# Kernel tuning notes

Measured on AMD Instinct MI355X. Metric: run time of the kernel, lower is better.

The kernel has to match this reference:

```python
import jax, jax.numpy as jnp
import numpy as np

B, L, D, V, K = 4, 2048, 1024, 32, 4096  # batch, seq, embedding_dim, vq_dim, num_embeddings


def setup_inputs() -> dict:
    key = jax.random.key(0)
    k0, k1, k2, k3 = jax.random.split(key, 4)
    h = jax.random.normal(k0, (B, L, D), jnp.float32)
    attn_mask = jnp.ones((B, L), jnp.float32)
    # proj: Linear(D -> V); proj_inv: Linear(V -> D)
    Wp = jax.random.normal(k1, (V, D), jnp.float32) / np.float32(np.sqrt(D))
    bp = jnp.zeros((V,), jnp.float32)
    Wpi = jax.random.normal(k2, (D, V), jnp.float32) / np.float32(np.sqrt(V))
    bpi = jnp.zeros((D,), jnp.float32)
    # embedding init uniform(-1/K, 1/K)
    emb = jax.random.uniform(k3, (K, V), jnp.float32, -1.0 / K, 1.0 / K)
    return {"h": h, "attn_mask": attn_mask, "Wp": Wp, "bp": bp,
            "Wpi": Wpi, "bpi": bpi, "emb": emb}


def reference(h, attn_mask, Wp, bp, Wpi, bpi, emb, temperature=1.0):
    # project + L2 normalize
    hp = jnp.einsum('bld,vd->blv', h, Wp) + bp            # [B,L,V]
    hp = hp / jnp.linalg.norm(hp, axis=-1, keepdims=True)
    # normalize codebook (in torch this is an in-place .data update)
    emb_n = emb / jnp.linalg.norm(emb, axis=-1, keepdims=True)  # [K,V]
    # squared euclidean distances hp vs codebook
    d = (jnp.sum(hp * hp, axis=-1, keepdims=True)
         + jnp.sum(emb_n * emb_n, axis=-1)
         - 2.0 * jnp.einsum('blv,kv->blk', hp, emb_n))    # [B,L,K]
    A = jax.nn.softmax(-d / temperature, axis=-1)         # [B,L,K]
    code = jnp.argmax(A, axis=-1)                         # [B,L]
    h_vq = jnp.einsum('blk,kv->blv', A, emb_n)            # train mode: A @ embedding
    # masked scatter into zeros is equivalent to masking out unselected positions
    m = (attn_mask == 1)
    quantized = jnp.where(m[..., None], h_vq, jnp.float32(0.0))
    vq_code = jnp.where(m, code, 0).astype(jnp.int32)
    quantized = jnp.einsum('blv,dv->bld', quantized, Wpi) + bpi
    vq_loss = jnp.float32(0.0)
    return quantized, vq_code, vq_loss
```

## Files before the change

### kernel.cpp

```cpp
#include <hip/hip_runtime.h>
#include <hip/hip_bf16.h>
#include <math.h>

#define NTOK 8192
#define DIM  1024
#define VDIM 32
#define KCODES 4096

#define SC 2.8853900817779268f

typedef __attribute__((ext_vector_type(8))) short short8;
typedef __attribute__((ext_vector_type(4))) float f32x4;

#define MFMA16(A,B,C) __builtin_amdgcn_mfma_f32_16x16x32_bf16(A, B, C, 0, 0, 0)

__device__ __forceinline__ unsigned short f2bf(float x) {
    unsigned u = __builtin_bit_cast(unsigned, x);
    u += 0x7FFF + ((u >> 16) & 1);
    return (unsigned short)(u >> 16);
}
__device__ __forceinline__ float bf2f(unsigned short b) {
    unsigned u = ((unsigned)b) << 16;
    return __builtin_bit_cast(float, u);
}
__device__ __forceinline__ float fexp2(float x) {
#if __has_builtin(__builtin_amdgcn_exp2f)
    return __builtin_amdgcn_exp2f(x);
#else
    return __expf(0.6931471805599453f * x);
#endif
}

struct U4 { unsigned x, y, z, w; };

__device__ __forceinline__ void split8(const float* p, short8* H, short8* L) {
    unsigned hh[4], ll[4];
    #pragma unroll
    for (int i = 0; i < 4; ++i) {
        unsigned short a = f2bf(p[2 * i]);
        unsigned short b = f2bf(p[2 * i + 1]);
        hh[i] = (unsigned)a | ((unsigned)b << 16);
        unsigned short la = f2bf(p[2 * i] - bf2f(a));
        unsigned short lb = f2bf(p[2 * i + 1] - bf2f(b));
        ll[i] = (unsigned)la | ((unsigned)lb << 16);
    }
    U4 uh = {hh[0], hh[1], hh[2], hh[3]};
    U4 ul = {ll[0], ll[1], ll[2], ll[3]};
    *H = __builtin_bit_cast(short8, uh);
    *L = __builtin_bit_cast(short8, ul);
}

__device__ __forceinline__ short8 pack8(const float* p) {
    unsigned u[8];
    #pragma unroll
    for (int j = 0; j < 8; ++j) u[j] = __builtin_bit_cast(unsigned, p[j]) + 0x8000u;
    U4 uh;
    uh.x = __builtin_amdgcn_perm(u[1], u[0], 0x07060302);
    uh.y = __builtin_amdgcn_perm(u[3], u[2], 0x07060302);
    uh.z = __builtin_amdgcn_perm(u[5], u[4], 0x07060302);
    uh.w = __builtin_amdgcn_perm(u[7], u[6], 0x07060302);
    return __builtin_bit_cast(short8, uh);
}

__device__ __forceinline__ int lsw(int row, int j) {
    int s = ((row >> 1) ^ (row >> 3)) & 3;
    return row * 40 + ((j ^ s) * 8);
}

#define OFS_E_HI   0
#define OFS_E_LO   131072
#define OFS_ET_HI  262144
#define OFS_WP_HI  393216
#define OFS_WP_LO  425984
#define OFS_WPI_HI 458752
#define OFS_WPI_LO 491520
#define OFS_HP_HI  524288
#define OFS_HP_LO  786432
#define F32_BASE   1048576
#define NSPLIT 8
#define FOFS_HVP 0
#define FOFS_LP  2097152
#define FOFS_AMP 2162688
#define FOFS_AIP 2228224

__global__ __launch_bounds__(256) void k_prep(const float* __restrict__ emb,
                                              const float* __restrict__ Wp,
                                              const float* __restrict__ Wpi,
                                              unsigned short* __restrict__ W,
                                              float* __restrict__ loss_out) {
    __shared__ __align__(16) unsigned short Th[32][72];
    int bid = blockIdx.x, tid = threadIdx.x;
    if (bid < 64) {
        int cb = bid * 64;
        int c = tid >> 2, s = tid & 3;
        const float* src = emb + (size_t)(cb + c) * VDIM + s * 8;
        float4 a = *(const float4*)src;
        float4 b = *(const float4*)(src + 4);
        float ps = a.x*a.x + a.y*a.y + a.z*a.z + a.w*a.w
                 + b.x*b.x + b.y*b.y + b.z*b.z + b.w*b.w;
        ps += __shfl_xor(ps, 1);
        ps += __shfl_xor(ps, 2);
        float inv = 1.0f / sqrtf(ps);
        float vals[8] = {a.x*inv, a.y*inv, a.z*inv, a.w*inv,
                         b.x*inv, b.y*inv, b.z*inv, b.w*inv};
        short8 H, L;
        split8(vals, &H, &L);
        *(short8*)(W + OFS_E_HI + (size_t)(cb + c) * VDIM + s * 8) = H;
        *(short8*)(W + OFS_E_LO + (size_t)(cb + c) * VDIM + s * 8) = L;
        #pragma unroll
        for (int j = 0; j < 8; ++j) Th[s * 8 + j][c] = f2bf(vals[j]);
        __syncthreads();
        int row = tid >> 3, seg = tid & 7;
        *(short8*)(W + OFS_ET_HI + (size_t)row * KCODES + cb + seg * 8) =
            *(const short8*)&Th[row][seg * 8];
        if (bid == 0 && tid == 0) loss_out[0] = 0.0f;
    } else if (bid < 80) {
        int i0 = (bid - 64) * 2048 + tid * 8;
        float4 a = *(const float4*)(Wp + i0);
        float4 b = *(const float4*)(Wp + i0 + 4);
        float vals[8] = {a.x, a.y, a.z, a.w, b.x, b.y, b.z, b.w};
        short8 H, L;
        split8(vals, &H, &L);
        *(short8*)(W + OFS_WP_HI + i0) = H;
        *(short8*)(W + OFS_WP_LO + i0) = L;
    } else {
        int i0 = (bid - 80) * 2048 + tid * 8;
        float4 a = *(const float4*)(Wpi + i0);
        float4 b = *(const float4*)(Wpi + i0 + 4);
        float vals[8] = {a.x, a.y, a.z, a.w, b.x, b.y, b.z, b.w};
        short8 H, L;
        split8(vals, &H, &L);
        *(short8*)(W + OFS_WPI_HI + i0) = H;
        *(short8*)(W + OFS_WPI_LO + i0) = L;
    }
}

__global__ __launch_bounds__(256) void k_proj(const float* __restrict__ h,
                                              const unsigned short* __restrict__ W,
                                              const float* __restrict__ bp,
                                              unsigned short* __restrict__ hp_hi,
                                              unsigned short* __restrict__ hp_lo) {
    __shared__ __align__(16) float red[4][16][36];
    const unsigned short* Wp_hi = W + OFS_WP_HI;
    const unsigned short* Wp_lo = W + OFS_WP_LO;
    int tid = threadIdx.x;
    int w = tid >> 6, l = tid & 63, q = l >> 4, m = l & 15;
    int tok0 = blockIdx.x * 16;
    const f32x4 zero4 = {0.f, 0.f, 0.f, 0.f};
    f32x4 acc0 = zero4, acc1 = zero4;
    const float* hb = h + (size_t)(tok0 + m) * DIM + w * 256 + q * 8;
    const unsigned short* w0h = Wp_hi + (size_t)m * DIM + w * 256 + q * 8;
    const unsigned short* w0l = Wp_lo + (size_t)m * DIM + w * 256 + q * 8;
    const unsigned short* w1h = w0h + (size_t)16 * DIM;
    const unsigned short* w1l = w0l + (size_t)16 * DIM;
    #pragma unroll
    for (int c = 0; c < 8; ++c) {
        float4 a = *(const float4*)(hb + c * 32);
        float4 b = *(const float4*)(hb + c * 32 + 4);
        float va[8] = {a.x, a.y, a.z, a.w, b.x, b.y, b.z, b.w};
        short8 Bh, Bl;
        split8(va, &Bh, &Bl);
        short8 A0h = *(const short8*)(w0h + c * 32);
        short8 A0l = *(const short8*)(w0l + c * 32);
        short8 A1h = *(const short8*)(w1h + c * 32);
        short8 A1l = *(const short8*)(w1l + c * 32);
        acc0 = MFMA16(A0l, Bl, acc0); acc0 = MFMA16(A0l, Bh, acc0);
        acc0 = MFMA16(A0h, Bl, acc0); acc0 = MFMA16(A0h, Bh, acc0);
        acc1 = MFMA16(A1l, Bl, acc1); acc1 = MFMA16(A1l, Bh, acc1);
        acc1 = MFMA16(A1h, Bl, acc1); acc1 = MFMA16(A1h, Bh, acc1);
    }
    *(f32x4*)&red[w][m][4 * q]      = acc0;
    *(f32x4*)&red[w][m][16 + 4 * q] = acc1;
    __syncthreads();
    #pragma unroll
    for (int half = 0; half < 2; ++half) {
        int t = (tid >> 5) + half * 8, v = tid & 31;
        float s = bp[v];
        #pragma unroll
        for (int j = 0; j < 4; ++j) s += red[j][t][v];
        float sq = s * s;
        #pragma unroll
        for (int off = 1; off < 32; off <<= 1) sq += __shfl_xor(sq, off);
        float nv = s * (SC / sqrtf(sq));
        unsigned short hb2 = f2bf(nv);
        size_t idx = (size_t)(tok0 + t) * VDIM + v;
        hp_hi[idx] = hb2;
        hp_lo[idx] = f2bf(nv - bf2f(hb2));
    }
}

__global__ __launch_bounds__(256, 4) void k_vq(const unsigned short* __restrict__ W,
                                               float* __restrict__ hvp,
                                               float* __restrict__ lp,
                                               float* __restrict__ amp,
                                               int* __restrict__ aip) {
    __shared__ __align__(16) unsigned short Eh[2][128 * 40];
    __shared__ __align__(16) unsigned short El[2][128 * 40];

    const unsigned short* E_hi  = W + OFS_E_HI;
    const unsigned short* E_lo  = W + OFS_E_LO;
    const unsigned short* Et_hi = W + OFS_ET_HI;
    const unsigned short* hp_hi = W + OFS_HP_HI;
    const unsigned short* hp_lo = W + OFS_HP_LO;

    int tid = threadIdx.x;
    int w = tid >> 6, l = tid & 63, q = l >> 4, m = l & 15;
    int tg = blockIdx.x >> 3, sp = blockIdx.x & 7;
    int tok0 = tg * 64 + w * 16;
    int cb0 = sp * 512;
    int sig = ((m & 12) << 1) | (m & 3);
    const f32x4 zero4 = {0.f, 0.f, 0.f, 0.f};

    int c0s = tid >> 2, j0s = tid & 3;
    int c1s = (tid + 256) >> 2, j1s = tid & 3;
    int ld0 = lsw(c0s, j0s), ld1 = lsw(c1s, j1s);
    size_t g0 = (size_t)c0s * VDIM + j0s * 8;
    size_t g1 = (size_t)c1s * VDIM + j1s * 8;

    size_t hidx = (size_t)(tok0 + m) * VDIM + q * 8;
    short8 hph = *(const short8*)(hp_hi + hidx);
    short8 hpl = *(const short8*)(hp_lo + hidx);

    {
        size_t tb = (size_t)cb0 * VDIM;
        short8 a0 = *(const short8*)(E_hi + tb + g0);
        short8 a1 = *(const short8*)(E_hi + tb + g1);
        short8 b0 = *(const short8*)(E_lo + tb + g0);
        short8 b1 = *(const short8*)(E_lo + tb + g1);
        *(short8*)&Eh[0][ld0] = a0;
        *(short8*)&Eh[0][ld1] = a1;
        *(short8*)&El[0][ld0] = b0;
        *(short8*)&El[0][ld1] = b1;
    }
    __syncthreads();

    f32x4 hv0 = zero4, hv1 = zero4;
    float ls = 0.f, am = -1e30f;
    int ai = 0;

    size_t tA = (size_t)sig * KCODES + cb0 + q * 8;
    short8 T0h = *(const short8*)(Et_hi + tA);
    short8 T1h = *(const short8*)(Et_hi + tA + (size_t)4 * KCODES);

    #pragma unroll 1
    for (int t = 0; t < 4; ++t) {
        int buf = t & 1;
        short8 sa0, sa1, sb0, sb1;
        if (t < 3) {
            size_t tb = (size_t)(cb0 + (t + 1) * 128) * VDIM;
            sa0 = *(const short8*)(E_hi + tb + g0);
            sa1 = *(const short8*)(E_hi + tb + g1);
            sb0 = *(const short8*)(E_lo + tb + g0);
            sb1 = *(const short8*)(E_lo + tb + g1);
        }
        #pragma unroll
        for (int cc = 0; cc < 4; ++cc) {
            int gch = t * 4 + cc;
            int cbase = cb0 + gch * 32;
            size_t tN = (size_t)sig * KCODES + (cbase + 32) + q * 8;
            short8 nT0h = *(const short8*)(Et_hi + tN);
            short8 nT1h = *(const short8*)(Et_hi + tN + (size_t)4 * KCODES);
            int r0 = cc * 32 + sig;
            short8 E0h = *(const short8*)&Eh[buf][lsw(r0, q)];
            short8 E0l = *(const short8*)&El[buf][lsw(r0, q)];
            short8 E1h = *(const short8*)&Eh[buf][lsw(r0 + 4, q)];
            short8 E1l = *(const short8*)&El[buf][lsw(r0 + 4, q)];

            f32x4 s0 = MFMA16(E0h, hpl, zero4);
            s0 = MFMA16(E0l, hph, s0);
            s0 = MFMA16(E0h, hph, s0);
            f32x4 s1 = MFMA16(E1h, hpl, zero4);
            s1 = MFMA16(E1l, hph, s1);
            s1 = MFMA16(E1h, hph, s1);

            float p[8];
            int lbase = cbase + 8 * q;
            #pragma unroll
            for (int r = 0; r < 4; ++r) {
                float sv = s0[r];
                if (sv > am) { am = sv; ai = lbase + r; }
                p[r] = fexp2(sv);
                sv = s1[r];
                if (sv > am) { am = sv; ai = lbase + 4 + r; }
                p[4 + r] = fexp2(sv);
            }
            ls += ((p[0] + p[1]) + (p[2] + p[3])) + ((p[4] + p[5]) + (p[6] + p[7]));
            short8 Ph = pack8(p);
            hv0 = MFMA16(T0h, Ph, hv0);
            hv1 = MFMA16(T1h, Ph, hv1);
            T0h = nT0h; T1h = nT1h;
        }
        if (t < 3) {
            int nb = buf ^ 1;
            *(short8*)&Eh[nb][ld0] = sa0;
            *(short8*)&Eh[nb][ld1] = sa1;
            *(short8*)&El[nb][ld0] = sb0;
            *(short8*)&El[nb][ld1] = sb1;
            __syncthreads();
        }
    }

    #pragma unroll
    for (int off = 16; off <= 32; off <<= 1) {
        ls += __shfl_xor(ls, off);
        float a2 = __shfl_xor(am, off);
        int   i2 = __shfl_xor(ai, off);
        if (a2 > am || (a2 == am && i2 < ai)) { am = a2; ai = i2; }
    }
    size_t gtok = (size_t)sp * NTOK + tok0;
    if (q == 0) {
        lp[gtok + m] = ls; amp[gtok + m] = am; aip[gtok + m] = ai;
    }
    float* dst = hvp + (gtok + m) * VDIM;
    *(f32x4*)(dst + 8 * q)     = hv0;
    *(f32x4*)(dst + 8 * q + 4) = hv1;
}

__global__ __launch_bounds__(256) void k_out(const unsigned short* __restrict__ W,
                                             const float* __restrict__ mask,
                                             const float* __restrict__ bpi,
                                             const float* __restrict__ hvp,
                                             const float* __restrict__ lp,
                                             const float* __restrict__ amp,
                                             const int* __restrict__ aip,
                                             float* __restrict__ out,
                                             float* __restrict__ code_out) {
    __shared__ float invl[16];
    __shared__ __align__(16) unsigned short hvh[16][40];
    __shared__ __align__(16) unsigned short hvl[16][40];
    const unsigned short* Wpi_hi = W + OFS_WPI_HI;
    const unsigned short* Wpi_lo = W + OFS_WPI_LO;
    int tid = threadIdx.x;
    int tok0 = blockIdx.x * 16;
    const f32x4 zero4 = {0.f, 0.f, 0.f, 0.f};

    if (tid < 16) {
        int tk = tok0 + tid;
        float L = 0.f, A = -1e30f;
        int I = 0x7fffffff;
        #pragma unroll
        for (int sp = 0; sp < NSPLIT; ++sp) {
            size_t gi = (size_t)sp * NTOK + tk;
            L += lp[gi];
            float a2 = amp[gi];
            int   i2 = aip[gi];
            if (a2 > A || (a2 == A && i2 < I)) { A = a2; I = i2; }
        }
        bool on = (mask[tk] == 1.0f);
        code_out[tk] = on ? (float)I : 0.0f;
        invl[tid] = on ? (1.0f / L) : 0.0f;
    }
    __syncthreads();
    #pragma unroll
    for (int it = 0; it < 2; ++it) {
        int idx = it * 256 + tid;
        int t = idx >> 5, v = idx & 31;
        float x = 0.f;
        #pragma unroll
        for (int sp = 0; sp < NSPLIT; ++sp)
            x += hvp[((size_t)sp * NTOK + tok0 + t) * VDIM + v];
        x *= invl[t];
        unsigned short hb = f2bf(x);
        hvh[t][v] = hb;
        hvl[t][v] = f2bf(x - bf2f(hb));
    }
    __syncthreads();
    int w = tid >> 6, l = tid & 63, q = l >> 4, m = l & 15;
    short8 gh = *(const short8*)&hvh[m][q * 8];
    short8 gl = *(const short8*)&hvl[m][q * 8];
    #pragma unroll
    for (int dt = 0; dt < 16; ++dt) {
        int dbase = w * 256 + dt * 16;
        short8 Ah = *(const short8*)(Wpi_hi + (size_t)(dbase + m) * VDIM + q * 8);
        short8 Al = *(const short8*)(Wpi_lo + (size_t)(dbase + m) * VDIM + q * 8);
        f32x4 o = MFMA16(Al, gh, zero4);
        o = MFMA16(Ah, gl, o);
        o = MFMA16(Ah, gh, o);
        float4 bias = *(const float4*)(bpi + dbase + 4 * q);
        float4 r0 = make_float4(o[0] + bias.x, o[1] + bias.y,
                                o[2] + bias.z, o[3] + bias.w);
        *(float4*)(out + (size_t)(tok0 + m) * DIM + dbase + 4 * q) = r0;
    }
}

extern "C" void kernel_launch(void* const* d_in, const int* in_sizes, int n_in,
                              void* d_out, int out_size, void* d_ws, size_t ws_size,
                              hipStream_t stream) {
    const float* h    = (const float*)d_in[0];
    const float* mask = (const float*)d_in[1];
    const float* Wp   = (const float*)d_in[2];
    const float* bp   = (const float*)d_in[3];
    const float* Wpi  = (const float*)d_in[4];
    const float* bpi  = (const float*)d_in[5];
    const float* emb  = (const float*)d_in[6];
    float* out = (float*)d_out;

    unsigned short* W = (unsigned short*)d_ws;
    unsigned short* hp_hi = W + OFS_HP_HI;
    unsigned short* hp_lo = W + OFS_HP_LO;
    float* fbase = (float*)(W + F32_BASE);
    float* hvp = fbase + FOFS_HVP;
    float* lpp = fbase + FOFS_LP;
    float* ampp = fbase + FOFS_AMP;
    int*   aipp = (int*)(fbase + FOFS_AIP);

    float* code_out = out + (size_t)NTOK * DIM;
    float* loss_out = code_out + NTOK;

    hipLaunchKernelGGL(k_prep, dim3(96),   dim3(256), 0, stream, emb, Wp, Wpi, W, loss_out);
    hipLaunchKernelGGL(k_proj, dim3(512),  dim3(256), 0, stream, h, W, bp, hp_hi, hp_lo);
    hipLaunchKernelGGL(k_vq,   dim3(1024), dim3(256), 0, stream, W, hvp, lpp, ampp, aipp);
    hipLaunchKernelGGL(k_out,  dim3(512),  dim3(256), 0, stream, W, mask, bpi, hvp, lpp, ampp, aipp, out, code_out);
}
```

Before: 148.8 us.

## Process two token tiles per wave in k_vq to reuse codebook fragments

Measured after the change: 136.4 us. -8.3%, faster.

```diff
diff --git a/kernel.cpp b/kernel.cpp
--- a/kernel.cpp
+++ b/kernel.cpp
@@ -189,13 +189,13 @@
     }
 }
 
-__global__ __launch_bounds__(256, 4) void k_vq(const unsigned short* __restrict__ W,
+__global__ __launch_bounds__(256, 2) void k_vq(const unsigned short* __restrict__ W,
                                                float* __restrict__ hvp,
                                                float* __restrict__ lp,
                                                float* __restrict__ amp,
                                                int* __restrict__ aip) {
-    __shared__ __align__(16) unsigned short Eh[2][128 * 40];
-    __shared__ __align__(16) unsigned short El[2][128 * 40];
+    __shared__ __align__(16) unsigned short Eh[2][64 * 40];
+    __shared__ __align__(16) unsigned short El[2][64 * 40];
 
     const unsigned short* E_hi  = W + OFS_E_HI;
     const unsigned short* E_lo  = W + OFS_E_LO;
@@ -206,57 +206,50 @@
     int tid = threadIdx.x;
     int w = tid >> 6, l = tid & 63, q = l >> 4, m = l & 15;
     int tg = blockIdx.x >> 3, sp = blockIdx.x & 7;
-    int tok0 = tg * 64 + w * 16;
+    int tok0 = tg * 128 + w * 32;
     int cb0 = sp * 512;
     int sig = ((m & 12) << 1) | (m & 3);
     const f32x4 zero4 = {0.f, 0.f, 0.f, 0.f};
 
-    int c0s = tid >> 2, j0s = tid & 3;
-    int c1s = (tid + 256) >> 2, j1s = tid & 3;
-    int ld0 = lsw(c0s, j0s), ld1 = lsw(c1s, j1s);
-    size_t g0 = (size_t)c0s * VDIM + j0s * 8;
-    size_t g1 = (size_t)c1s * VDIM + j1s * 8;
-
-    size_t hidx = (size_t)(tok0 + m) * VDIM + q * 8;
-    short8 hph = *(const short8*)(hp_hi + hidx);
-    short8 hpl = *(const short8*)(hp_lo + hidx);
+    int cs = tid >> 2, js = tid & 3;
+    int lds_off = lsw(cs, js);
+    size_t gs = (size_t)cs * VDIM + js * 8;
+
+    size_t h0 = (size_t)(tok0 + m) * VDIM + q * 8;
+    short8 hph0 = *(const short8*)(hp_hi + h0);
+    short8 hpl0 = *(const short8*)(hp_lo + h0);
+    short8 hph1 = *(const short8*)(hp_hi + h0 + 16 * VDIM);
+    short8 hpl1 = *(const short8*)(hp_lo + h0 + 16 * VDIM);
 
     {
         size_t tb = (size_t)cb0 * VDIM;
-        short8 a0 = *(const short8*)(E_hi + tb + g0);
-        short8 a1 = *(const short8*)(E_hi + tb + g1);
-        short8 b0 = *(const short8*)(E_lo + tb + g0);
-        short8 b1 = *(const short8*)(E_lo + tb + g1);
-        *(short8*)&Eh[0][ld0] = a0;
-        *(short8*)&Eh[0][ld1] = a1;
-        *(short8*)&El[0][ld0] = b0;
-        *(short8*)&El[0][ld1] = b1;
+        short8 a = *(const short8*)(E_hi + tb + gs);
+        short8 b = *(const short8*)(E_lo + tb + gs);
+        *(short8*)&Eh[0][lds_off] = a;
+        *(short8*)&El[0][lds_off] = b;
     }
     __syncthreads();
 
-    f32x4 hv0 = zero4, hv1 = zero4;
-    float ls = 0.f, am = -1e30f;
-    int ai = 0;
+    f32x4 hv00 = zero4, hv01 = zero4, hv10 = zero4, hv11 = zero4;
+    float ls0 = 0.f, ls1 = 0.f, am0 = -1e30f, am1 = -1e30f;
+    int ai0 = 0, ai1 = 0;
 
     size_t tA = (size_t)sig * KCODES + cb0 + q * 8;
     short8 T0h = *(const short8*)(Et_hi + tA);
     short8 T1h = *(const short8*)(Et_hi + tA + (size_t)4 * KCODES);
 
     #pragma unroll 1
-    for (int t = 0; t < 4; ++t) {
+    for (int t = 0; t < 8; ++t) {
         int buf = t & 1;
-        short8 sa0, sa1, sb0, sb1;
-        if (t < 3) {
-            size_t tb = (size_t)(cb0 + (t + 1) * 128) * VDIM;
-            sa0 = *(const short8*)(E_hi + tb + g0);
-            sa1 = *(const short8*)(E_hi + tb + g1);
-            sb0 = *(const short8*)(E_lo + tb + g0);
-            sb1 = *(const short8*)(E_lo + tb + g1);
+        short8 sa, sb;
+        if (t < 7) {
+            size_t tb = (size_t)(cb0 + (t + 1) * 64) * VDIM;
+            sa = *(const short8*)(E_hi + tb + gs);
+            sb = *(const short8*)(E_lo + tb + gs);
         }
         #pragma unroll
-        for (int cc = 0; cc < 4; ++cc) {
-            int gch = t * 4 + cc;
-            int cbase = cb0 + gch * 32;
+        for (int cc = 0; cc < 2; ++cc) {
+            int cbase = cb0 + t * 64 + cc * 32;
             size_t tN = (size_t)sig * KCODES + (cbase + 32) + q * 8;
             short8 nT0h = *(const short8*)(Et_hi + tN);
             short8 nT1h = *(const short8*)(Et_hi + tN + (size_t)4 * KCODES);
@@ -265,55 +258,84 @@
             short8 E0l = *(const short8*)&El[buf][lsw(r0, q)];
             short8 E1h = *(const short8*)&Eh[buf][lsw(r0 + 4, q)];
             short8 E1l = *(const short8*)&El[buf][lsw(r0 + 4, q)];
-
-            f32x4 s0 = MFMA16(E0h, hpl, zero4);
-            s0 = MFMA16(E0l, hph, s0);
-            s0 = MFMA16(E0h, hph, s0);
-            f32x4 s1 = MFMA16(E1h, hpl, zero4);
-            s1 = MFMA16(E1l, hph, s1);
-            s1 = MFMA16(E1h, hph, s1);
-
-            float p[8];
             int lbase = cbase + 8 * q;
-            #pragma unroll
-            for (int r = 0; r < 4; ++r) {
-                float sv = s0[r];
-                if (sv > am) { am = sv; ai = lbase + r; }
-                p[r] = fexp2(sv);
-                sv = s1[r];
-                if (sv > am) { am = sv; ai = lbase + 4 + r; }
-                p[4 + r] = fexp2(sv);
+
+            {
+                f32x4 s0 = MFMA16(E0h, hpl0, zero4);
+                s0 = MFMA16(E0l, hph0, s0);
+                s0 = MFMA16(E0h, hph0, s0);
+                f32x4 s1 = MFMA16(E1h, hpl0, zero4);
+                s1 = MFMA16(E1l, hph0, s1);
+                s1 = MFMA16(E1h, hph0, s1);
+                float p[8];
+                #pragma unroll
+                for (int r = 0; r < 4; ++r) {
+                    float sv = s0[r];
+                    if (sv > am0) { am0 = sv; ai0 = lbase + r; }
+                    p[r] = fexp2(sv);
+                    sv = s1[r];
+                    if (sv > am0) { am0 = sv; ai0 = lbase + 4 + r; }
+                    p[4 + r] = fexp2(sv);
+                }
+                ls0 += ((p[0] + p[1]) + (p[2] + p[3])) + ((p[4] + p[5]) + (p[6] + p[7]));
+                short8 Ph = pack8(p);
+                hv00 = MFMA16(T0h, Ph, hv00);
+                hv01 = MFMA16(T1h, Ph, hv01);
             }
-            ls += ((p[0] + p[1]) + (p[2] + p[3])) + ((p[4] + p[5]) + (p[6] + p[7]));
-            short8 Ph = pack8(p);
-            hv0 = MFMA16(T0h, Ph, hv0);
-            hv1 = MFMA16(T1h, Ph, hv1);
+            {
+                f32x4 s0 = MFMA16(E0h, hpl1, zero4);
+                s0 = MFMA16(E0l, hph1, s0);
+                s0 = MFMA16(E0h, hph1, s0);
+                f32x4 s1 = MFMA16(E1h, hpl1, zero4);
+                s1 = MFMA16(E1l, hph1, s1);
+                s1 = MFMA16(E1h, hph1, s1);
+                float p[8];
+                #pragma unroll
+                for (int r = 0; r < 4; ++r) {
+                    float sv = s0[r];
+                    if (sv > am1) { am1 = sv; ai1 = lbase + r; }
+                    p[r] = fexp2(sv);
+                    sv = s1[r];
+                    if (sv > am1) { am1 = sv; ai1 = lbase + 4 + r; }
+                    p[4 + r] = fexp2(sv);
+                }
+                ls1 += ((p[0] + p[1]) + (p[2] + p[3])) + ((p[4] + p[5]) + (p[6] + p[7]));
+                short8 Ph = pack8(p);
+                hv10 = MFMA16(T0h, Ph, hv10);
+                hv11 = MFMA16(T1h, Ph, hv11);
+            }
             T0h = nT0h; T1h = nT1h;
         }
-        if (t < 3) {
+        if (t < 7) {
             int nb = buf ^ 1;
-            *(short8*)&Eh[nb][ld0] = sa0;
-            *(short8*)&Eh[nb][ld1] = sa1;
-            *(short8*)&El[nb][ld0] = sb0;
-            *(short8*)&El[nb][ld1] = sb1;
+            *(short8*)&Eh[nb][lds_off] = sa;
+            *(short8*)&El[nb][lds_off] = sb;
             __syncthreads();
         }
     }
 
     #pragma unroll
     for (int off = 16; off <= 32; off <<= 1) {
-        ls += __shfl_xor(ls, off);
-        float a2 = __shfl_xor(am, off);
-        int   i2 = __shfl_xor(ai, off);
-        if (a2 > am || (a2 == am && i2 < ai)) { am = a2; ai = i2; }
+        ls0 += __shfl_xor(ls0, off);
+        float a2 = __shfl_xor(am0, off);
+        int   i2 = __shfl_xor(ai0, off);
+        if (a2 > am0 || (a2 == am0 && i2 < ai0)) { am0 = a2; ai0 = i2; }
+        ls1 += __shfl_xor(ls1, off);
+        a2 = __shfl_xor(am1, off);
+        i2 = __shfl_xor(ai1, off);
+        if (a2 > am1 || (a2 == am1 && i2 < ai1)) { am1 = a2; ai1 = i2; }
     }
     size_t gtok = (size_t)sp * NTOK + tok0;
     if (q == 0) {
-        lp[gtok + m] = ls; amp[gtok + m] = am; aip[gtok + m] = ai;
-    }
-    float* dst = hvp + (gtok + m) * VDIM;
-    *(f32x4*)(dst + 8 * q)     = hv0;
-    *(f32x4*)(dst + 8 * q + 4) = hv1;
+        lp[gtok + m] = ls0;      amp[gtok + m] = am0;      aip[gtok + m] = ai0;
+        lp[gtok + 16 + m] = ls1; amp[gtok + 16 + m] = am1; aip[gtok + 16 + m] = ai1;
+    }
+    float* dst0 = hvp + (gtok + m) * VDIM;
+    *(f32x4*)(dst0 + 8 * q)     = hv00;
+    *(f32x4*)(dst0 + 8 * q + 4) = hv01;
+    float* dst1 = hvp + (gtok + 16 + m) * VDIM;
+    *(f32x4*)(dst1 + 8 * q)     = hv10;
+    *(f32x4*)(dst1 + 8 * q + 4) = hv11;
 }
 
 __global__ __launch_bounds__(256) void k_out(const unsigned short* __restrict__ W,
@@ -407,8 +429,8 @@
     float* code_out = out + (size_t)NTOK * DIM;
     float* loss_out = code_out + NTOK;
 
-    hipLaunchKernelGGL(k_prep, dim3(96),   dim3(256), 0, stream, emb, Wp, Wpi, W, loss_out);
-    hipLaunchKernelGGL(k_proj, dim3(512),  dim3(256), 0, stream, h, W, bp, hp_hi, hp_lo);
-    hipLaunchKernelGGL(k_vq,   dim3(1024), dim3(256), 0, stream, W, hvp, lpp, ampp, aipp);
-    hipLaunchKernelGGL(k_out,  dim3(512),  dim3(256), 0, stream, W, mask, bpi, hvp, lpp, ampp, aipp, out, code_out);
-}
+    hipLaunchKernelGGL(k_prep, dim3(96),  dim3(256), 0, stream, emb, Wp, Wpi, W, loss_out);
+    hipLaunchKernelGGL(k_proj, dim3(512), dim3(256), 0, stream, h, W, bp, hp_hi, hp_lo);
+    hipLaunchKernelGGL(k_vq,   dim3(512), dim3(256), 0, stream, W, hvp, lpp, ampp, aipp);
+    hipLaunchKernelGGL(k_out,  dim3(512), dim3(256), 0, stream, W, mask, bpi, hvp, lpp, ampp, aipp, out, code_out);
+}
```

## Register-tile four token tiles per wave in VQ kernel and double code splits

Applied to the files above, without the earlier changes.

Measured after the change: 141.4 us. 1.05x faster.

```diff
diff --git a/kernel.cpp b/kernel.cpp
--- a/kernel.cpp
+++ b/kernel.cpp
@@ -77,11 +77,11 @@
 #define OFS_HP_HI  524288
 #define OFS_HP_LO  786432
 #define F32_BASE   1048576
-#define NSPLIT 8
+#define NSPLIT 16
 #define FOFS_HVP 0
-#define FOFS_LP  2097152
-#define FOFS_AMP 2162688
-#define FOFS_AIP 2228224
+#define FOFS_LP  4194304
+#define FOFS_AMP 4325376
+#define FOFS_AIP 4456448
 
 __global__ __launch_bounds__(256) void k_prep(const float* __restrict__ emb,
                                               const float* __restrict__ Wp,
@@ -189,13 +189,13 @@
     }
 }
 
-__global__ __launch_bounds__(256, 4) void k_vq(const unsigned short* __restrict__ W,
+__global__ __launch_bounds__(128, 2) void k_vq(const unsigned short* __restrict__ W,
                                                float* __restrict__ hvp,
                                                float* __restrict__ lp,
                                                float* __restrict__ amp,
                                                int* __restrict__ aip) {
-    __shared__ __align__(16) unsigned short Eh[2][128 * 40];
-    __shared__ __align__(16) unsigned short El[2][128 * 40];
+    __shared__ __align__(16) unsigned short Eh[2][64 * 40];
+    __shared__ __align__(16) unsigned short El[2][64 * 40];
 
     const unsigned short* E_hi  = W + OFS_E_HI;
     const unsigned short* E_lo  = W + OFS_E_LO;
@@ -205,38 +205,46 @@
 
     int tid = threadIdx.x;
     int w = tid >> 6, l = tid & 63, q = l >> 4, m = l & 15;
-    int tg = blockIdx.x >> 3, sp = blockIdx.x & 7;
-    int tok0 = tg * 64 + w * 16;
-    int cb0 = sp * 512;
+    int tg = blockIdx.x >> 4, sp = blockIdx.x & 15;
+    int tok0 = tg * 128 + w * 64;
+    int cb0 = sp * 256;
     int sig = ((m & 12) << 1) | (m & 3);
     const f32x4 zero4 = {0.f, 0.f, 0.f, 0.f};
 
-    int c0s = tid >> 2, j0s = tid & 3;
-    int c1s = (tid + 256) >> 2, j1s = tid & 3;
-    int ld0 = lsw(c0s, j0s), ld1 = lsw(c1s, j1s);
-    size_t g0 = (size_t)c0s * VDIM + j0s * 8;
-    size_t g1 = (size_t)c1s * VDIM + j1s * 8;
-
-    size_t hidx = (size_t)(tok0 + m) * VDIM + q * 8;
-    short8 hph = *(const short8*)(hp_hi + hidx);
-    short8 hpl = *(const short8*)(hp_lo + hidx);
+    int cs = tid >> 1, js = tid & 1;
+    int ldA = lsw(cs, js), ldB = lsw(cs, js + 2);
+    size_t gA = (size_t)cs * VDIM + js * 8;
+    size_t gB = gA + 16;
+
+    size_t h0 = (size_t)(tok0 + m) * VDIM + q * 8;
+    short8 hph[4], hpl[4];
+    #pragma unroll
+    for (int tl = 0; tl < 4; ++tl) {
+        hph[tl] = *(const short8*)(hp_hi + h0 + tl * 16 * VDIM);
+        hpl[tl] = *(const short8*)(hp_lo + h0 + tl * 16 * VDIM);
+    }
 
     {
         size_t tb = (size_t)cb0 * VDIM;
-        short8 a0 = *(const short8*)(E_hi + tb + g0);
-        short8 a1 = *(const short8*)(E_hi + tb + g1);
-        short8 b0 = *(const short8*)(E_lo + tb + g0);
-        short8 b1 = *(const short8*)(E_lo + tb + g1);
-        *(short8*)&Eh[0][ld0] = a0;
-        *(short8*)&Eh[0][ld1] = a1;
-        *(short8*)&El[0][ld0] = b0;
-        *(short8*)&El[0][ld1] = b1;
+        short8 a0 = *(const short8*)(E_hi + tb + gA);
+        short8 a1 = *(const short8*)(E_hi + tb + gB);
+        short8 b0 = *(const short8*)(E_lo + tb + gA);
+        short8 b1 = *(const short8*)(E_lo + tb + gB);
+        *(short8*)&Eh[0][ldA] = a0;
+        *(short8*)&Eh[0][ldB] = a1;
+        *(short8*)&El[0][ldA] = b0;
+        *(short8*)&El[0][ldB] = b1;
     }
     __syncthreads();
 
-    f32x4 hv0 = zero4, hv1 = zero4;
-    float ls = 0.f, am = -1e30f;
-    int ai = 0;
+    f32x4 hv0[4], hv1[4];
+    float ls[4], am[4];
+    int ai[4];
+    #pragma unroll
+    for (int tl = 0; tl < 4; ++tl) {
+        hv0[tl] = zero4; hv1[tl] = zero4;
+        ls[tl] = 0.f; am[tl] = -1e30f; ai[tl] = 0;
+    }
 
     size_t tA = (size_t)sig * KCODES + cb0 + q * 8;
     short8 T0h = *(const short8*)(Et_hi + tA);
@@ -247,16 +255,15 @@
         int buf = t & 1;
         short8 sa0, sa1, sb0, sb1;
         if (t < 3) {
-            size_t tb = (size_t)(cb0 + (t + 1) * 128) * VDIM;
-            sa0 = *(const short8*)(E_hi + tb + g0);
-            sa1 = *(const short8*)(E_hi + tb + g1);
-            sb0 = *(const short8*)(E_lo + tb + g0);
-            sb1 = *(const short8*)(E_lo + tb + g1);
-        }
-        #pragma unroll
-        for (int cc = 0; cc < 4; ++cc) {
-            int gch = t * 4 + cc;
-            int cbase = cb0 + gch * 32;
+            size_t tb = (size_t)(cb0 + (t + 1) * 64) * VDIM;
+            sa0 = *(const short8*)(E_hi + tb + gA);
+            sa1 = *(const short8*)(E_hi + tb + gB);
+            sb0 = *(const short8*)(E_lo + tb + gA);
+            sb1 = *(const short8*)(E_lo + tb + gB);
+        }
+        #pragma unroll
+        for (int cc = 0; cc < 2; ++cc) {
+            int cbase = cb0 + t * 64 + cc * 32;
             size_t tN = (size_t)sig * KCODES + (cbase + 32) + q * 8;
             short8 nT0h = *(const short8*)(Et_hi + tN);
             short8 nT1h = *(const short8*)(Et_hi + tN + (size_t)4 * KCODES);
@@ -265,55 +272,69 @@
             short8 E0l = *(const short8*)&El[buf][lsw(r0, q)];
             short8 E1h = *(const short8*)&Eh[buf][lsw(r0 + 4, q)];
             short8 E1l = *(const short8*)&El[buf][lsw(r0 + 4, q)];
-
-            f32x4 s0 = MFMA16(E0h, hpl, zero4);
-            s0 = MFMA16(E0l, hph, s0);
-            s0 = MFMA16(E0h, hph, s0);
-            f32x4 s1 = MFMA16(E1h, hpl, zero4);
-            s1 = MFMA16(E1l, hph, s1);
-            s1 = MFMA16(E1h, hph, s1);
-
-            float p[8];
             int lbase = cbase + 8 * q;
+
             #pragma unroll
-            for (int r = 0; r < 4; ++r) {
-                float sv = s0[r];
-                if (sv > am) { am = sv; ai = lbase + r; }
-                p[r] = fexp2(sv);
-                sv = s1[r];
-                if (sv > am) { am = sv; ai = lbase + 4 + r; }
-                p[4 + r] = fexp2(sv);
+            for (int tl = 0; tl < 4; ++tl) {
+                f32x4 s0 = MFMA16(E0h, hpl[tl], zero4);
+                s0 = MFMA16(E0l, hph[tl], s0);
+                s0 = MFMA16(E0h, hph[tl], s0);
+                f32x4 s1 = MFMA16(E1h, hpl[tl], zero4);
+                s1 = MFMA16(E1l, hph[tl], s1);
+                s1 = MFMA16(E1h, hph[tl], s1);
+                float p[8];
+                #pragma unroll
+                for (int r = 0; r < 4; ++r) {
+                    float sv = s0[r];
+                    if (sv > am[tl]) { am[tl] = sv; ai[tl] = lbase + r; }
+                    p[r] = fexp2(sv);
+                    sv = s1[r];
+                    if (sv > am[tl]) { am[tl] = sv; ai[tl] = lbase + 4 + r; }
+                    p[4 + r] = fexp2(sv);
+                }
+                ls[tl] += ((p[0] + p[1]) + (p[2] + p[3]))
+                        + ((p[4] + p[5]) + (p[6] + p[7]));
+                short8 Ph = pack8(p);
+                hv0[tl] = MFMA16(T0h, Ph, hv0[tl]);
+                hv1[tl] = MFMA16(T1h, Ph, hv1[tl]);
             }
-            ls += ((p[0] + p[1]) + (p[2] + p[3])) + ((p[4] + p[5]) + (p[6] + p[7]));
-            short8 Ph = pack8(p);
-            hv0 = MFMA16(T0h, Ph, hv0);
-            hv1 = MFMA16(T1h, Ph, hv1);
             T0h = nT0h; T1h = nT1h;
         }
         if (t < 3) {
             int nb = buf ^ 1;
-            *(short8*)&Eh[nb][ld0] = sa0;
-            *(short8*)&Eh[nb][ld1] = sa1;
-            *(short8*)&El[nb][ld0] = sb0;
-            *(short8*)&El[nb][ld1] = sb1;
+            *(short8*)&Eh[nb][ldA] = sa0;
+            *(short8*)&Eh[nb][ldB] = sa1;
+            *(short8*)&El[nb][ldA] = sb0;
+            *(short8*)&El[nb][ldB] = sb1;
             __syncthreads();
         }
     }
 
     #pragma unroll
-    for (int off = 16; off <= 32; off <<= 1) {
-        ls += __shfl_xor(ls, off);
-        float a2 = __shfl_xor(am, off);
-        int   i2 = __shfl_xor(ai, off);
-        if (a2 > am || (a2 == am && i2 < ai)) { am = a2; ai = i2; }
+    for (int tl = 0; tl < 4; ++tl) {
+        #pragma unroll
+        for (int off = 16; off <= 32; off <<= 1) {
+            ls[tl] += __shfl_xor(ls[tl], off);
+            float a2 = __shfl_xor(am[tl], off);
+            int   i2 = __shfl_xor(ai[tl], off);
+            if (a2 > am[tl] || (a2 == am[tl] && i2 < ai[tl])) { am[tl] = a2; ai[tl] = i2; }
+        }
     }
     size_t gtok = (size_t)sp * NTOK + tok0;
     if (q == 0) {
-        lp[gtok + m] = ls; amp[gtok + m] = am; aip[gtok + m] = ai;
-    }
-    float* dst = hvp + (gtok + m) * VDIM;
-    *(f32x4*)(dst + 8 * q)     = hv0;
-    *(f32x4*)(dst + 8 * q + 4) = hv1;
+        #pragma unroll
+        for (int tl = 0; tl < 4; ++tl) {
+            lp[gtok + tl * 16 + m] = ls[tl];
+            amp[gtok + tl * 16 + m] = am[tl];
+            aip[gtok + tl * 16 + m] = ai[tl];
+        }
+    }
+    #pragma unroll
+    for (int tl = 0; tl < 4; ++tl) {
+        float* dst = hvp + (gtok + tl * 16 + m) * VDIM;
+        *(f32x4*)(dst + 8 * q)     = hv0[tl];
+        *(f32x4*)(dst + 8 * q + 4) = hv1[tl];
+    }
 }
 
 __global__ __launch_bounds__(256) void k_out(const unsigned short* __restrict__ W,
@@ -409,6 +430,6 @@
 
     hipLaunchKernelGGL(k_prep, dim3(96),   dim3(256), 0, stream, emb, Wp, Wpi, W, loss_out);
     hipLaunchKernelGGL(k_proj, dim3(512),  dim3(256), 0, stream, h, W, bp, hp_hi, hp_lo);
-    hipLaunchKernelGGL(k_vq,   dim3(1024), dim3(256), 0, stream, W, hvp, lpp, ampp, aipp);
+    hipLaunchKernelGGL(k_vq,   dim3(1024), dim3(128), 0, stream, W, hvp, lpp, ampp, aipp);
     hipLaunchKernelGGL(k_out,  dim3(512),  dim3(256), 0, stream, W, mask, bpi, hvp, lpp, ampp, aipp, out, code_out);
 }
```
